# Performance work log

Measured on AMD Instinct MI355X. Metric: run time of the kernel, lower is better.

Reference implementation:

```python
import jax, jax.numpy as jnp
import numpy as np

N_OPS = 32
D_REASON = 128
TOP_K = 2
EPS = 1e-05
LEAK = 1e-05  # coefficient on the all-ops leak term


def setup_inputs() -> dict:
    key = jax.random.key(0)
    k1, k2, k3, k4 = jax.random.split(key, 4)
    B, S = 8, 2048
    x = jax.random.normal(k1, (B, S, D_REASON), dtype=jnp.float32)
    indices = jax.random.randint(k2, (B, S, TOP_K), 0, N_OPS, dtype=jnp.int64)
    weights = jax.random.uniform(k3, (B, S, TOP_K), dtype=jnp.float32)
    ops = 0.02 * jax.random.normal(k4, (N_OPS, D_REASON, D_REASON), dtype=jnp.float32)
    return {"x": x, "indices": indices, "weights": weights, "ops": ops}


def _ternary_effective(ops):
    # scale_n = clamp(mean|W_n|, 1e-5); q = STE ternary quantize; W_eff = q * scale
    scale = jnp.maximum(jnp.mean(jnp.abs(ops), axis=(1, 2)), EPS)  # (N,)
    q_hard = jnp.clip(jnp.round(ops / scale[:, None, None]), -1.0, 1.0)
    # STE: identity gradient w.r.t. ops through the quantizer
    q = ops + jax.lax.stop_gradient(q_hard - ops)
    return q * scale[:, None, None]  # (N, D, D)


def reference(x, indices, weights, ops):
    # x: (B,S,D); indices: (B,S,K) int; weights: (B,S,K); ops: (N,D,D)
    w_eff = _ternary_effective(ops)  # (N, D_out, D_in)
    # F.linear(x, W) = x @ W.T, for every op at once -> T: (B,S,N,D_out)
    T = jnp.einsum("bsd,nod->bsno", x, w_eff)
    total = T.sum(axis=2)  # sum over all ops, (B,S,D)
    # gather the selected top_k ops per token: (B,S,K,D)
    gathered = jnp.take_along_axis(T, indices[..., None].astype(jnp.int32), axis=2)
    routed = jnp.sum(weights[..., None] * gathered, axis=2)  # (B,S,D)
    return LEAK * total / N_OPS + routed
```

## Files before the change

kernel.cpp:

```cpp
#include <hip/hip_runtime.h>

#define N_OPS 32
#define D 128
#define MAT (D * D)
#define EPS 1e-5f
#define NTOK (8 * 2048)
#define NASSIGN (NTOK * 2)
#define CAP 40960
#define EXP_BLKS (CAP / 256)

typedef __attribute__((ext_vector_type(8))) short short8;
typedef __attribute__((ext_vector_type(4))) float f32x4;

__device__ inline unsigned short f2bf(float f) {
    unsigned int u = __float_as_uint(f);
    return (unsigned short)((u + 0x7FFF + ((u >> 16) & 1)) >> 16);
}
__device__ inline float bf2f(unsigned short h) {
    return __uint_as_float(((unsigned int)h) << 16);
}

__global__ __launch_bounds__(256) void k_prep(const float* __restrict__ ops,
                                              const int* __restrict__ idx,
                                              float* __restrict__ scale,
                                              int* __restrict__ hist2,
                                              unsigned short* __restrict__ wb) {
    if (blockIdx.x < N_OPS) {
        const int e = blockIdx.x;
        const float* W = ops + e * MAT;
        float s = 0.f;
        for (int i = threadIdx.x; i < MAT; i += 256) s += fabsf(W[i]);
        for (int off = 32; off; off >>= 1) s += __shfl_xor(s, off);
        __shared__ float red[4];
        __shared__ float s_scale;
        const int lane = threadIdx.x & 63, wid = threadIdx.x >> 6;
        if (lane == 0) red[wid] = s;
        __syncthreads();
        if (threadIdx.x == 0) {
            s_scale = fmaxf((red[0] + red[1] + red[2] + red[3]) / (float)MAT, EPS);
            scale[e] = s_scale;
        }
        __syncthreads();
        const float sc = s_scale;
#pragma unroll
        for (int it = 0; it < 8; ++it) {
            const int f = it * 256 + threadIdx.x;
            const int o = f >> 4, dc = f & 15;
            const float4* wp = (const float4*)(W + o * D + dc * 8);
            float4 a = wp[0], b = wp[1];
            float v[8] = {a.x, a.y, a.z, a.w, b.x, b.y, b.z, b.w};
            unsigned short q[8];
#pragma unroll
            for (int j = 0; j < 8; ++j) {
                float t = rintf(v[j] / sc);
                t = fminf(1.f, fmaxf(-1.f, t));
                q[j] = (t == 0.f) ? 0 : (t > 0.f ? 0x3F80 : 0xBF80);
            }
            ((short8*)wb)[e * 2048 + dc * 128 + o] = *(const short8*)q;
        }
    } else {
        const int b = blockIdx.x - N_OPS;
        __shared__ int lh[N_OPS];
        if (threadIdx.x < N_OPS) lh[threadIdx.x] = 0;
        __syncthreads();
#pragma unroll
        for (int j = 0; j < 4; ++j)
            atomicAdd(&lh[idx[b * 1024 + j * 256 + threadIdx.x]], 1);
        __syncthreads();
        if (threadIdx.x < N_OPS) hist2[b * N_OPS + threadIdx.x] = lh[threadIdx.x];
    }
}

__global__ __launch_bounds__(256) void k_scatter(const int* __restrict__ idx,
                                                 const int* __restrict__ hist2,
                                                 int* __restrict__ list) {
    const int b = blockIdx.x;
    __shared__ int hl[1024];
    __shared__ int stot[N_OPS];
    __shared__ int soff[N_OPS + 1];
    __shared__ int sbase[N_OPS];
    __shared__ int lh[N_OPS];
    for (int i = threadIdx.x; i < 1024; i += 256) hl[i] = hist2[i];
    if (threadIdx.x < N_OPS) lh[threadIdx.x] = 0;
    __syncthreads();
    if (threadIdx.x < N_OPS) {
        int t = 0;
        for (int b2 = 0; b2 < 32; ++b2) t += hl[b2 * N_OPS + threadIdx.x];
        stot[threadIdx.x] = t;
    }
    __syncthreads();
    if (threadIdx.x == 0) {
        int run = 0;
        for (int e = 0; e < N_OPS; ++e) { soff[e] = run; run += (stot[e] + 255) & ~255; }
        soff[N_OPS] = run;
    }
    __syncthreads();
    if (threadIdx.x < N_OPS) {
        const int e = threadIdx.x;
        int r = soff[e];
        for (int b2 = 0; b2 < b; ++b2) r += hl[b2 * N_OPS + e];
        sbase[e] = r;
    }
    __syncthreads();
#pragma unroll
    for (int j = 0; j < 4; ++j) {
        const int a = b * 1024 + j * 256 + threadIdx.x;
        const int e = idx[a];
        const int r = atomicAdd(&lh[e], 1);
        list[sbase[e] + r] = (e << 20) | a;
    }
    for (int s = soff[b] + stot[b] + (int)threadIdx.x; s < soff[b + 1]; s += 256)
        list[s] = -1;
    if (b == 0)
        for (int s = soff[N_OPS] + (int)threadIdx.x; s < CAP; s += 256) list[s] = -1;
}

__global__ __launch_bounds__(256, 2) void k_mfma(const float* __restrict__ x,
                                                 const int* __restrict__ list,
                                                 const unsigned short* __restrict__ wb,
                                                 const float* __restrict__ scale,
                                                 unsigned short* __restrict__ part2) {
    __shared__ short8 lB[2048];
    const int lane = threadIdx.x & 63;
    const int wv   = threadIdx.x >> 6;
    const int quad = lane >> 4;
    const int ncol = lane & 15;

    const int base = blockIdx.x * 256;
    const int v0 = list[base];
    if (v0 < 0) return;
    const int e = v0 >> 20;
    const short8* src = (const short8*)wb + e * 2048;
    const float sc = scale[e];

    for (int i = threadIdx.x; i < 2048; i += 256) lB[i] = src[i];
    __syncthreads();

    for (int g = 0; g < 4; ++g) {
        const int rowbase = base + g * 64 + wv * 16;
        const int v = list[rowbase + ncol];
        const int tok = (v < 0) ? 0 : ((v & 0xFFFFF) >> 1);
        const float4* Xp = (const float4*)(x + (size_t)tok * D);

        f32x4 acc[8];
#pragma unroll
        for (int j = 0; j < 8; ++j) acc[j] = (f32x4){0.f, 0.f, 0.f, 0.f};

#pragma unroll
        for (int s = 0; s < 4; ++s) {
            const float4 xa = Xp[(s * 32 + quad * 8) >> 2];
            const float4 xb4 = Xp[((s * 32 + quad * 8) >> 2) + 1];
            unsigned short af[8] = {f2bf(xa.x), f2bf(xa.y), f2bf(xa.z), f2bf(xa.w),
                                    f2bf(xb4.x), f2bf(xb4.y), f2bf(xb4.z), f2bf(xb4.w)};
            const short8 a = *(const short8*)af;
            const short8* Bp = lB + (s * 4 + quad) * 128;
#pragma unroll
            for (int nt = 0; nt < 8; ++nt) {
                const short8 b = Bp[nt * 16 + ncol];
                acc[nt] = __builtin_amdgcn_mfma_f32_16x16x32_bf16(a, b, acc[nt], 0, 0, 0);
            }
        }
#pragma unroll
        for (int r = 0; r < 4; ++r) {
            const int vr = list[rowbase + quad * 4 + r];
            if (vr < 0) continue;
            unsigned short* dst = part2 + (size_t)(vr & 0xFFFFF) * D;
#pragma unroll
            for (int nt = 0; nt < 8; ++nt)
                dst[nt * 16 + ncol] = f2bf(acc[nt][r] * sc);
        }
    }
}

__global__ __launch_bounds__(256) void k_final(const unsigned short* __restrict__ part2,
                                               const float* __restrict__ wts,
                                               float* __restrict__ out) {
    const int lane = threadIdx.x & 63;
#pragma unroll
    for (int it = 0; it < 8; ++it) {
        const int t = __builtin_amdgcn_readfirstlane(
            blockIdx.x * 32 + it * 4 + (threadIdx.x >> 6));
        const float w0 = wts[2 * t], w1 = wts[2 * t + 1];
        const unsigned int a0 = ((const unsigned int*)(part2 + (size_t)(2 * t) * D))[lane];
        const unsigned int a1 = ((const unsigned int*)(part2 + (size_t)(2 * t + 1) * D))[lane];
        float2 o;
        o.x = w0 * bf2f((unsigned short)(a0 & 0xFFFF))
            + w1 * bf2f((unsigned short)(a1 & 0xFFFF));
        o.y = w0 * bf2f((unsigned short)(a0 >> 16))
            + w1 * bf2f((unsigned short)(a1 >> 16));
        ((float2*)out)[(size_t)t * 64 + lane] = o;
    }
}

extern "C" void kernel_launch(void* const* d_in, const int* in_sizes, int n_in,
                              void* d_out, int out_size, void* d_ws, size_t ws_size,
                              hipStream_t stream) {
    const float* x   = (const float*)d_in[0];
    const int*   idx = (const int*)  d_in[1];
    const float* wts = (const float*)d_in[2];
    const float* ops = (const float*)d_in[3];
    float* out = (float*)d_out;

    unsigned short* part2 = (unsigned short*)d_ws;
    unsigned short* wb    = part2 + (size_t)NASSIGN * D;
    float*          scale = (float*)(wb + N_OPS * MAT);
    int*            hist2 = (int*)(scale + 32);
    int*            list  = hist2 + 1024;

    k_prep<<<64, 256, 0, stream>>>(ops, idx, scale, hist2, wb);
    k_scatter<<<32, 256, 0, stream>>>(idx, hist2, list);
    k_mfma<<<EXP_BLKS, 256, 0, stream>>>(x, list, wb, scale, part2);
    k_final<<<NTOK / 32, 256, 0, stream>>>(part2, wts, out);
}
```

Measured before the change: 106.0 us.

## Fuse histogram and scatter into prep kernel, shrink expert tiles to 128 rows

Drops the separate scatter kernel. Each of the 32 routing blocks in the prep kernel now scans all 32768 indices itself to get the global per-op totals and its own prefix counts, then writes its slice of the sorted assignment list directly. This removes one launch and one global round-trip through the histogram buffer, at the cost of redundant index reads in every block. Expert segments are now padded to 128 instead of 256, and the MFMA kernel handles 128 rows per block. That cuts wasted padded rows and raises the block count, but each block now loads the 32 KB weight tile to LDS for half as many rows.

```diff
diff --git a/kernel.cpp b/kernel.cpp
--- a/kernel.cpp
+++ b/kernel.cpp
@@ -6,8 +6,8 @@
 #define EPS 1e-5f
 #define NTOK (8 * 2048)
 #define NASSIGN (NTOK * 2)
-#define CAP 40960
-#define EXP_BLKS (CAP / 256)
+#define CAP 36864
+#define EXP_BLKS (CAP / 128)
 
 typedef __attribute__((ext_vector_type(8))) short short8;
 typedef __attribute__((ext_vector_type(4))) float f32x4;
@@ -23,20 +23,21 @@
 __global__ __launch_bounds__(256) void k_prep(const float* __restrict__ ops,
                                               const int* __restrict__ idx,
                                               float* __restrict__ scale,
-                                              int* __restrict__ hist2,
-                                              unsigned short* __restrict__ wb) {
+                                              unsigned short* __restrict__ wb,
+                                              int* __restrict__ list) {
+    const int tid = threadIdx.x;
     if (blockIdx.x < N_OPS) {
         const int e = blockIdx.x;
         const float* W = ops + e * MAT;
         float s = 0.f;
-        for (int i = threadIdx.x; i < MAT; i += 256) s += fabsf(W[i]);
+        for (int i = tid; i < MAT; i += 256) s += fabsf(W[i]);
         for (int off = 32; off; off >>= 1) s += __shfl_xor(s, off);
         __shared__ float red[4];
         __shared__ float s_scale;
-        const int lane = threadIdx.x & 63, wid = threadIdx.x >> 6;
+        const int lane = tid & 63, wid = tid >> 6;
         if (lane == 0) red[wid] = s;
         __syncthreads();
-        if (threadIdx.x == 0) {
+        if (tid == 0) {
             s_scale = fmaxf((red[0] + red[1] + red[2] + red[3]) / (float)MAT, EPS);
             scale[e] = s_scale;
         }
@@ -44,7 +45,7 @@
         const float sc = s_scale;
 #pragma unroll
         for (int it = 0; it < 8; ++it) {
-            const int f = it * 256 + threadIdx.x;
+            const int f = it * 256 + tid;
             const int o = f >> 4, dc = f & 15;
             const float4* wp = (const float4*)(W + o * D + dc * 8);
             float4 a = wp[0], b = wp[1];
@@ -60,59 +61,37 @@
         }
     } else {
         const int b = blockIdx.x - N_OPS;
+        __shared__ int tot[N_OPS];
+        __shared__ int pre[N_OPS];
         __shared__ int lh[N_OPS];
-        if (threadIdx.x < N_OPS) lh[threadIdx.x] = 0;
+        __shared__ int soff[N_OPS + 1];
+        if (tid < N_OPS) { tot[tid] = 0; pre[tid] = 0; lh[tid] = 0; }
+        __syncthreads();
+        const int cut = b * 1024;
+        for (int a = tid; a < NASSIGN; a += 256) {
+            const int e = idx[a];
+            atomicAdd(&tot[e], 1);
+            if (a < cut) atomicAdd(&pre[e], 1);
+        }
+        __syncthreads();
+        if (tid == 0) {
+            int run = 0;
+            for (int e = 0; e < N_OPS; ++e) { soff[e] = run; run += (tot[e] + 127) & ~127; }
+            soff[N_OPS] = run;
+        }
         __syncthreads();
 #pragma unroll
-        for (int j = 0; j < 4; ++j)
-            atomicAdd(&lh[idx[b * 1024 + j * 256 + threadIdx.x]], 1);
-        __syncthreads();
-        if (threadIdx.x < N_OPS) hist2[b * N_OPS + threadIdx.x] = lh[threadIdx.x];
+        for (int j = 0; j < 4; ++j) {
+            const int a = cut + j * 256 + tid;
+            const int e = idx[a];
+            const int r = atomicAdd(&lh[e], 1);
+            list[soff[e] + pre[e] + r] = (e << 20) | a;
+        }
+        for (int s = soff[b] + tot[b] + tid; s < soff[b + 1]; s += 256)
+            list[s] = -1;
+        if (b == 0)
+            for (int s = soff[N_OPS] + tid; s < CAP; s += 256) list[s] = -1;
     }
-}
-
-__global__ __launch_bounds__(256) void k_scatter(const int* __restrict__ idx,
-                                                 const int* __restrict__ hist2,
-                                                 int* __restrict__ list) {
-    const int b = blockIdx.x;
-    __shared__ int hl[1024];
-    __shared__ int stot[N_OPS];
-    __shared__ int soff[N_OPS + 1];
-    __shared__ int sbase[N_OPS];
-    __shared__ int lh[N_OPS];
-    for (int i = threadIdx.x; i < 1024; i += 256) hl[i] = hist2[i];
-    if (threadIdx.x < N_OPS) lh[threadIdx.x] = 0;
-    __syncthreads();
-    if (threadIdx.x < N_OPS) {
-        int t = 0;
-        for (int b2 = 0; b2 < 32; ++b2) t += hl[b2 * N_OPS + threadIdx.x];
-        stot[threadIdx.x] = t;
-    }
-    __syncthreads();
-    if (threadIdx.x == 0) {
-        int run = 0;
-        for (int e = 0; e < N_OPS; ++e) { soff[e] = run; run += (stot[e] + 255) & ~255; }
-        soff[N_OPS] = run;
-    }
-    __syncthreads();
-    if (threadIdx.x < N_OPS) {
-        const int e = threadIdx.x;
-        int r = soff[e];
-        for (int b2 = 0; b2 < b; ++b2) r += hl[b2 * N_OPS + e];
-        sbase[e] = r;
-    }
-    __syncthreads();
-#pragma unroll
-    for (int j = 0; j < 4; ++j) {
-        const int a = b * 1024 + j * 256 + threadIdx.x;
-        const int e = idx[a];
-        const int r = atomicAdd(&lh[e], 1);
-        list[sbase[e] + r] = (e << 20) | a;
-    }
-    for (int s = soff[b] + stot[b] + (int)threadIdx.x; s < soff[b + 1]; s += 256)
-        list[s] = -1;
-    if (b == 0)
-        for (int s = soff[N_OPS] + (int)threadIdx.x; s < CAP; s += 256) list[s] = -1;
 }
 
 __global__ __launch_bounds__(256, 2) void k_mfma(const float* __restrict__ x,
@@ -126,7 +105,7 @@
     const int quad = lane >> 4;
     const int ncol = lane & 15;
 
-    const int base = blockIdx.x * 256;
+    const int base = blockIdx.x * 128;
     const int v0 = list[base];
     if (v0 < 0) return;
     const int e = v0 >> 20;
@@ -136,7 +115,7 @@
     for (int i = threadIdx.x; i < 2048; i += 256) lB[i] = src[i];
     __syncthreads();
 
-    for (int g = 0; g < 4; ++g) {
+    for (int g = 0; g < 2; ++g) {
         const int rowbase = base + g * 64 + wv * 16;
         const int v = list[rowbase + ncol];
         const int tok = (v < 0) ? 0 : ((v & 0xFFFFF) >> 1);
@@ -148,7 +127,7 @@
 
 #pragma unroll
         for (int s = 0; s < 4; ++s) {
-            const float4 xa = Xp[(s * 32 + quad * 8) >> 2];
+            const float4 xa  = Xp[(s * 32 + quad * 8) >> 2];
             const float4 xb4 = Xp[((s * 32 + quad * 8) >> 2) + 1];
             unsigned short af[8] = {f2bf(xa.x), f2bf(xa.y), f2bf(xa.z), f2bf(xa.w),
                                     f2bf(xb4.x), f2bf(xb4.y), f2bf(xb4.z), f2bf(xb4.w)};
@@ -204,11 +183,9 @@
     unsigned short* part2 = (unsigned short*)d_ws;
     unsigned short* wb    = part2 + (size_t)NASSIGN * D;
     float*          scale = (float*)(wb + N_OPS * MAT);
-    int*            hist2 = (int*)(scale + 32);
-    int*            list  = hist2 + 1024;
+    int*            list  = (int*)(scale + 32);
 
-    k_prep<<<64, 256, 0, stream>>>(ops, idx, scale, hist2, wb);
-    k_scatter<<<32, 256, 0, stream>>>(idx, hist2, list);
+    k_prep<<<64, 256, 0, stream>>>(ops, idx, scale, wb, list);
     k_mfma<<<EXP_BLKS, 256, 0, stream>>>(x, list, wb, scale, part2);
     k_final<<<NTOK / 32, 256, 0, stream>>>(part2, wts, out);
 }
```

Result: slower. 116.4 us (+9.7%).
